# Performance work log

Hardware: AMD Instinct MI355X
Metric: run time of the kernel (lower is better)

## Reference

```python
import jax, jax.numpy as jnp
import numpy as np

PI = float(np.pi)
BN_EPS = 1e-3
LN_EPS = 1e-5


def ssslu(x, shape, bias):
    # x * (sin(softsign(x) * shape*pi/2) + (bias + 1))
    s = x / (1.0 + jnp.abs(x))
    return x * (jnp.sin(s * (shape * PI / 2.0)) + (bias + 1.0))


def bn(x, g, b, m, v):
    inv = (g / jnp.sqrt(v + BN_EPS))[None, :, None, None]
    return (x - m[None, :, None, None]) * inv + b[None, :, None, None]


def conv2d(x, w, bias=None, pad=0):
    y = jax.lax.conv_general_dilated(x, w, (1, 1), [(pad, pad), (pad, pad)],
                                     dimension_numbers=('NCHW', 'OIHW', 'NCHW'))
    if bias is not None:
        y = y + bias[None, :, None, None]
    return y


def ln_silu(v):
    # LayerNorm (unit weight, zero bias) over last axis, then SiLU
    mu = jnp.mean(v, axis=-1, keepdims=True)
    var = jnp.mean(jnp.square(v - mu), axis=-1, keepdims=True)
    h = (v - mu) / jnp.sqrt(var + LN_EPS)
    return h * jax.nn.sigmoid(h)


def _forward(x, w_qkv, g_qkv, b_qkv, m_qkv, v_qkv,
             w_co, g_co, b_co, m_co, v_co,
             w_b1, bias_b1, g_b1, b_b1, m_b1, v_b1,
             w_b2, bias_b2, g_b2, b_b2, m_b2, v_b2):
    B, C, H, W = x.shape
    Q = (w_qkv.shape[0] - C) // 2
    # qkv Conv block: conv1x1 -> SSSLU(-3, 0.3) -> BN
    t = bn(ssslu(conv2d(x, w_qkv, pad=0), -3.0, 0.3), g_qkv, b_qkv, m_qkv, v_qkv)
    xq, xk, xv = jnp.split(t, [Q, 2 * Q], axis=1)
    # max-pooled Q/K rows and columns -> [B*Q, W] / [B*Q, H]
    qw = jnp.max(xq, axis=2).reshape(B * Q, W)
    kw = jnp.max(xk, axis=2).reshape(B * Q, W)
    qh = jnp.max(xq, axis=3).reshape(B * Q, H)
    kh = jnp.max(xk, axis=3).reshape(B * Q, H)
    # xaw[i,b] = max_a qw[i,a]*kw[i,b]; xah[i,a] = max_b qh[i,a]*kh[i,b]
    xaw = jnp.max(qw[:, :, None] * kw[:, None, :], axis=1)  # [BQ, W]
    xah = jnp.max(qh[:, :, None] * kh[:, None, :], axis=2)  # [BQ, H]
    xaw = ln_silu(xaw)
    xah = ln_silu(xah)
    xa = (xah[:, :, None] * xaw[:, None, :]).reshape(B, Q, H, W)
    # co: SSSLUConv(Q+C -> Q): conv3x3 -> BN -> SSSLU(1.0, 0)
    xa = jnp.concatenate([xa, xv], axis=1)
    xa = ssslu(bn(conv2d(xa, w_co, pad=1), g_co, b_co, m_co, v_co), 1.0, 0.0)
    # back[0]: Conv(Q -> C, k3, bias): conv -> SSSLU(-3, 0.3) -> BN
    xa = bn(ssslu(conv2d(xa, w_b1, bias_b1, pad=1), -3.0, 0.3), g_b1, b_b1, m_b1, v_b1)
    # back[1]: SSSLUConv(C -> C, k1, bias): conv -> BN -> SSSLU(0.8, 0)
    xa = ssslu(bn(conv2d(xa, w_b2, bias_b2, pad=0), g_b2, b_b2, m_b2, v_b2), 0.8, 0.0)
    # back[2]: Sigmoid; source returns the gate itself
    return jax.nn.sigmoid(xa)


def setup_inputs() -> dict:
    B, C, Q, H, W = 16, 256, 256, 64, 64
    key = jax.random.key(0)
    ks = jax.random.split(key, 32)

    def w_init(k, o, i, kh, kw):
        return jax.random.normal(k, (o, i, kh, kw), jnp.float32) * (1.0 / np.sqrt(i * kh * kw))

    def bn_params(k, c):
        k1, k2, k3, k4 = jax.random.split(k, 4)
        g = jax.random.uniform(k1, (c,), jnp.float32, 0.5, 1.5)
        b = jax.random.normal(k2, (c,), jnp.float32) * 0.1
        m = jax.random.normal(k3, (c,), jnp.float32) * 0.1
        v = jax.random.uniform(k4, (c,), jnp.float32, 0.5, 1.5)
        return g, b, m, v

    x = jax.random.normal(ks[0], (B, C, H, W), jnp.float32)
    w_qkv = w_init(ks[1], 2 * Q + C, C, 1, 1)
    g_qkv, b_qkv, m_qkv, v_qkv = bn_params(ks[2], 2 * Q + C)
    w_co = w_init(ks[3], Q, Q + C, 3, 3)
    g_co, b_co, m_co, v_co = bn_params(ks[4], Q)
    w_b1 = w_init(ks[5], C, Q, 3, 3)
    bias_b1 = jax.random.normal(ks[6], (C,), jnp.float32) * 0.05
    g_b1, b_b1, m_b1, v_b1 = bn_params(ks[7], C)
    w_b2 = w_init(ks[8], C, C, 1, 1)
    bias_b2 = jax.random.normal(ks[9], (C,), jnp.float32) * 0.05
    g_b2, b_b2, m_b2, v_b2 = bn_params(ks[10], C)
    return dict(x=x, w_qkv=w_qkv, g_qkv=g_qkv, b_qkv=b_qkv, m_qkv=m_qkv, v_qkv=v_qkv,
                w_co=w_co, g_co=g_co, b_co=b_co, m_co=m_co, v_co=v_co,
                w_b1=w_b1, bias_b1=bias_b1, g_b1=g_b1, b_b1=b_b1, m_b1=m_b1, v_b1=v_b1,
                w_b2=w_b2, bias_b2=bias_b2, g_b2=g_b2, b_b2=b_b2, m_b2=m_b2, v_b2=v_b2)


def reference(x, w_qkv, g_qkv, b_qkv, m_qkv, v_qkv,
              w_co, g_co, b_co, m_co, v_co,
              w_b1, bias_b1, g_b1, b_b1, m_b1, v_b1,
              w_b2, bias_b2, g_b2, b_b2, m_b2, v_b2):
    return _forward(x, w_qkv, g_qkv, b_qkv, m_qkv, v_qkv,
                    w_co, g_co, b_co, m_co, v_co,
                    w_b1, bias_b1, g_b1, b_b1, m_b1, v_b1,
                    w_b2, bias_b2, g_b2, b_b2, m_b2, v_b2)
```

## Files before the change

kernel.cpp:

```cpp
#include <hip/hip_runtime.h>
#include <hip/hip_bf16.h>
#include <math.h>

#define PI_F 3.14159265358979323846f

typedef unsigned short u16;
typedef unsigned int   u32;
typedef float    f32x4 __attribute__((ext_vector_type(4)));
typedef _Float16 f16x8 __attribute__((ext_vector_type(8)));
typedef u16      u16x8 __attribute__((ext_vector_type(8)));

__device__ __forceinline__ u16 f2h(float f){ union{ _Float16 h; u16 u; } c; c.h = (_Float16)f; return c.u; }
__device__ __forceinline__ float h2f(u16 u){ union{ u16 u; _Float16 h; } c; c.u = u; return (float)c.h; }

__device__ __forceinline__ void gl16(const void* g, void* l){
  __builtin_amdgcn_global_load_lds((const __attribute__((address_space(1))) u32*)g,
                                   (__attribute__((address_space(3))) u32*)l, 16, 0, 0);
}

__device__ __forceinline__ int SWZ(int r){ return (r>>1)&3; }

__device__ __forceinline__ float wred_max(float v){
#pragma unroll
  for (int m = 32; m; m >>= 1) v = fmaxf(v, __shfl_xor(v, m));
  return v;
}
__device__ __forceinline__ float wred_min(float v){
#pragma unroll
  for (int m = 32; m; m >>= 1) v = fminf(v, __shfl_xor(v, m));
  return v;
}
__device__ __forceinline__ float wred_sum(float v){
#pragma unroll
  for (int m = 32; m; m >>= 1) v += __shfl_xor(v, m);
  return v;
}

__device__ __forceinline__ float ssslu_f(float x, float shp, float bp1){
  float s = x / (1.0f + fabsf(x));
  return x * (__sinf(s * shp) + bp1);
}

__device__ __forceinline__ float epi_val(float v, float4 p, float shp, float bp1, int ORDER, bool SIG){
  v += p.w;
  if (ORDER == 0){ v = ssslu_f(v, shp, bp1); v = (v - p.z) * p.x + p.y; }
  else           { v = (v - p.z) * p.x + p.y; v = ssslu_f(v, shp, bp1); }
  if (SIG) v = 1.f / (1.f + __expf(-v));
  return v;
}

__device__ __forceinline__ void atomicMaxF(float* a, float v){
  if (v >= 0.f) atomicMax(reinterpret_cast<int*>(a), __float_as_int(v));
  else          atomicMin(reinterpret_cast<unsigned int*>(a), __float_as_uint(v));
}

__device__ __forceinline__ f16x8 mul8h(u16x8 a, u16x8 b){
  union{ u16x8 u; f16x8 h; } A, B; A.u = a; B.u = b;
  return A.h * B.h;
}

template<int CI_T, bool CAT>
__global__ __launch_bounds__(512, 2)
void conv3_mfma(const u16* __restrict__ Apk, const u16* __restrict__ Bg,
                u16* __restrict__ DstH, const float4* __restrict__ pp,
                const u16* __restrict__ xahT_, const u16* __restrict__ xawT_,
                float shp, float bp1, int ORDER)
{
  constexpr int NCC = CI_T / 32;
  constexpr int NIT = NCC * 3;
  __shared__ __align__(16) u16 sAB[73728];

  const int tid  = threadIdx.x;
  const int lane = tid & 63;
  const int wv   = tid >> 6;
  const int wm   = wv >> 2;
  const int wn   = wv & 3;
  const int l15  = lane & 15, l4 = lane >> 4;

  const int bx  = blockIdx.x;
  const int bid = (bx & 7) * 32 + (bx >> 3);
  const int b   = bid >> 4;
  const int r0  = (bid & 15) * 4;

  auto STAGE = [&](int it2){
    int d2 = it2 % 3, c2 = it2 / 3;
    if (d2 == 0){
      int bufB = c2 & 1;
#pragma unroll
      for (int j = 0; j < 3; ++j){
        int rr  = 2 * j + (tid >> 8);
        int hh  = r0 - 1 + rr; hh = min(63, max(0, hh));
        int rem = tid & 255;
        int w   = rem >> 2, s = rem & 3;
        int ci0 = c2 * 32 + ((s ^ SWZ(w + 1)) << 3);
        if (CAT && c2 < 8){
          u16x8 vh = *(const u16x8*)&xahT_[((b * 64 + hh) << 8) + ci0];
          u16x8 vw = *(const u16x8*)&xawT_[((b * 64 + w ) << 8) + ci0];
          *(f16x8*)&sAB[49152 + bufB * 12288 + rr * 2048 + w * 32 + s * 8] = mul8h(vh, vw);
        } else {
          int ci = CAT ? (ci0 - 256) : ci0;
          const u16* src = Bg + (((size_t)b * 4096 + hh * 64 + w) << 8) + ci;
          gl16(src, &sAB[49152 + bufB * 12288 + rr * 2048 + (wv & 3) * 512]);
        }
      }
    }
    int bufA = it2 & 1;
#pragma unroll
    for (int j2 = 0; j2 < 3; ++j2){
      int tap = d2 * 3 + j2;
      const u16* base = Apk + (size_t)tap * 256 * CI_T + c2 * 32;
#pragma unroll
      for (int i = 0; i < 2; ++i){
        int row = i * 128 + (tid >> 2);
        int s   = tid & 3;
        const u16* src = base + (size_t)row * CI_T + ((s ^ SWZ(row)) << 3);
        gl16(src, &sAB[bufA * 24576 + j2 * 8192 + (i * 128 + wv * 16) * 32]);
      }
    }
  };

  f32x4 acc[8][4];
#pragma unroll
  for (int i = 0; i < 8; ++i)
#pragma unroll
    for (int j = 0; j < 4; ++j){ acc[i][j][0]=0.f; acc[i][j][1]=0.f; acc[i][j][2]=0.f; acc[i][j][3]=0.f; }

  STAGE(0);
  __syncthreads();

  for (int it = 0; it < NIT; ++it){
    if (it + 1 < NIT) STAGE(it + 1);

    const int d = it % 3, c = it / 3;
    const int bufA = it & 1, bufB = c & 1;
    const int brow = wn + d;
    const bool rowok = ((unsigned)(r0 + wn + d - 1)) < 64u;

#pragma unroll
    for (int dw = 0; dw < 3; ++dw){
      f16x8 afr[8], bfr[4];
#pragma unroll
      for (int fm = 0; fm < 8; ++fm){
        int m  = wm * 128 + fm * 16 + l15;
        int sl = l4 ^ SWZ(m);
        afr[fm] = *(const f16x8*)&sAB[bufA * 24576 + dw * 8192 + m * 32 + sl * 8];
      }
#pragma unroll
      for (int fn = 0; fn < 4; ++fn){
        int w_in = fn * 16 + l15 + dw - 1;
        int wc   = min(63, max(0, w_in));
        int sl2  = l4 ^ SWZ(wc + 1);
        f16x8 t  = *(const f16x8*)&sAB[49152 + bufB * 12288 + brow * 2048 + wc * 32 + sl2 * 8];
        bool ok  = rowok && (((unsigned)w_in) < 64u);
        bfr[fn]  = ok ? t : (f16x8)(_Float16)0;
      }
      __builtin_amdgcn_s_setprio(1);
#pragma unroll
      for (int fm = 0; fm < 8; ++fm)
#pragma unroll
        for (int fn = 0; fn < 4; ++fn)
          acc[fm][fn] = __builtin_amdgcn_mfma_f32_16x16x32_f16(afr[fm], bfr[fn], acc[fm][fn], 0, 0, 0);
      __builtin_amdgcn_s_setprio(0);
    }
    __syncthreads();
  }

  const int h = r0 + wn;
#pragma unroll
  for (int fm = 0; fm < 8; ++fm){
    const int cobase = wm * 128 + fm * 16 + 4 * l4;
    float4 P0 = pp[cobase], P1 = pp[cobase+1], P2 = pp[cobase+2], P3 = pp[cobase+3];
#pragma unroll
    for (int fn = 0; fn < 4; ++fn){
      int w = fn * 16 + l15;
      float v0 = epi_val(acc[fm][fn][0], P0, shp, bp1, ORDER, false);
      float v1 = epi_val(acc[fm][fn][1], P1, shp, bp1, ORDER, false);
      float v2 = epi_val(acc[fm][fn][2], P2, shp, bp1, ORDER, false);
      float v3 = epi_val(acc[fm][fn][3], P3, shp, bp1, ORDER, false);
      uint2 st;
      st.x = (u32)f2h(v0) | ((u32)f2h(v1) << 16);
      st.y = (u32)f2h(v2) | ((u32)f2h(v3) << 16);
      *(uint2*)&DstH[(((size_t)b * 4096 + (size_t)h * 64 + w) << 8) + cobase] = st;
    }
  }
}

template<int SRC, int EPI, int HLOOP>
__global__ __launch_bounds__(256)
void conv_mfma(const u16* __restrict__ Apk, const u16* __restrict__ Bg,
               u16* __restrict__ DstH, float* __restrict__ DstF,
               const float4* __restrict__ pp,
               const float* __restrict__ Xf,
               float* __restrict__ qwp, float* __restrict__ kwp,
               float* __restrict__ qhp, float* __restrict__ khp,
               float shp, float bp1, int ORDER, int M)
{
  constexpr int NCC = 8;
  __shared__ __align__(16) u16 sA[2][8192];
  __shared__ __align__(16) u16 sB[2][2112];

  const int tid  = threadIdx.x;
  const int lane = tid & 63;
  const int wv   = tid >> 6;
  const int bx   = blockIdx.x;
  const int b    = (HLOOP == 8) ? (bx >> 3) : (bx >> 6);
  const int h0   = (HLOOP == 8) ? ((bx & 7) * 8) : (bx & 63);
  const int m0   = blockIdx.y * 256;

  f32x4 acc[4][4];
  f32x4 cmax[4][4];
  if (EPI == 0){
#pragma unroll
    for (int i = 0; i < 4; ++i)
#pragma unroll
      for (int j = 0; j < 4; ++j){ cmax[i][j][0]=-3.0e38f; cmax[i][j][1]=-3.0e38f; cmax[i][j][2]=-3.0e38f; cmax[i][j][3]=-3.0e38f; }
  }

  for (int hi = 0; hi < HLOOP; ++hi){
    const int h = h0 + hi;
#pragma unroll
    for (int i = 0; i < 4; ++i)
#pragma unroll
      for (int j = 0; j < 4; ++j){ acc[i][j][0]=0.f; acc[i][j][1]=0.f; acc[i][j][2]=0.f; acc[i][j][3]=0.f; }

    auto stageA = [&](int c, int buf){
      const u16* base = Apk + (size_t)m0 * 256 + c * 32;
#pragma unroll
      for (int i = 0; i < 4; ++i){
        int row = i * 64 + (tid >> 2);
        int s   = tid & 3;
        const u16* src = base + (size_t)row * 256 + ((s ^ SWZ(row)) << 3);
        gl16(src, &sA[buf][(i * 64 + wv * 16) * 32]);
      }
    };
    auto stageB = [&](int c, int buf){
      const int w = tid >> 2, s = tid & 3, r = w + 1;
      if (SRC == 0){
        int ci0 = c * 32 + ((s ^ SWZ(r)) << 3);
        const float* xp = Xf + ((size_t)(b * 256 + ci0)) * 4096 + h * 64 + w;
        u16x8 v;
#pragma unroll
        for (int j = 0; j < 8; ++j) v[j] = f2h(xp[(size_t)j * 4096]);
        *(u16x8*)&sB[buf][r * 32 + s * 8] = v;
      } else {
        const u16* src = Bg + (((size_t)b * 4096 + h * 64 + w) << 8) + c * 32 + ((s ^ SWZ(r)) << 3);
        gl16(src, &sB[buf][(1 + wv * 16) * 32]);
      }
    };

    __syncthreads();
    stageA(0, 0);
    stageB(0, 0);
    __syncthreads();

    for (int it = 0; it < NCC; ++it){
      if (it + 1 < NCC){ stageA(it + 1, (it + 1) & 1); stageB(it + 1, (it + 1) & 1); }
      f16x8 afr[4], bfr[4];
#pragma unroll
      for (int fm = 0; fm < 4; ++fm){
        int row = wv * 64 + fm * 16 + (lane & 15);
        int sl  = (lane >> 4) ^ SWZ(row);
        afr[fm] = *(const f16x8*)&sA[it & 1][row * 32 + sl * 8];
      }
#pragma unroll
      for (int fn = 0; fn < 4; ++fn){
        int r  = fn * 16 + (lane & 15) + 1;
        int sl = (lane >> 4) ^ SWZ(r);
        bfr[fn] = *(const f16x8*)&sB[it & 1][r * 32 + sl * 8];
      }
      __builtin_amdgcn_s_setprio(1);
#pragma unroll
      for (int fm = 0; fm < 4; ++fm)
#pragma unroll
        for (int fn = 0; fn < 4; ++fn)
          acc[fm][fn] = __builtin_amdgcn_mfma_f32_16x16x32_f16(afr[fm], bfr[fn], acc[fm][fn], 0, 0, 0);
      __builtin_amdgcn_s_setprio(0);
      __syncthreads();
    }

    const int l15 = lane & 15, l4 = lane >> 4;
    if (EPI == 0){
#pragma unroll
      for (int fm = 0; fm < 4; ++fm){
        const int cobase = m0 + wv * 64 + fm * 16 + 4 * l4;
        float4 P0 = pp[cobase], P1 = pp[cobase+1], P2 = pp[cobase+2], P3 = pp[cobase+3];
        f32x4 ev[4];
#pragma unroll
        for (int fn = 0; fn < 4; ++fn){
          ev[fn][0] = epi_val(acc[fm][fn][0], P0, shp, bp1, ORDER, false);
          ev[fn][1] = epi_val(acc[fm][fn][1], P1, shp, bp1, ORDER, false);
          ev[fn][2] = epi_val(acc[fm][fn][2], P2, shp, bp1, ORDER, false);
          ev[fn][3] = epi_val(acc[fm][fn][3], P3, shp, bp1, ORDER, false);
#pragma unroll
          for (int r = 0; r < 4; ++r) cmax[fm][fn][r] = fmaxf(cmax[fm][fn][r], ev[fn][r]);
        }
#pragma unroll
        for (int r = 0; r < 4; ++r){
          float mv = fmaxf(fmaxf(ev[0][r], ev[1][r]), fmaxf(ev[2][r], ev[3][r]));
          mv = fmaxf(mv, __shfl_xor(mv, 1));
          mv = fmaxf(mv, __shfl_xor(mv, 2));
          mv = fmaxf(mv, __shfl_xor(mv, 4));
          mv = fmaxf(mv, __shfl_xor(mv, 8));
          if (l15 == 0){
            int q = (cobase + r) & 255;
            float* rowp = (m0 == 0) ? qhp : khp;
            rowp[(((b << 8) | q) << 6) + h] = mv;
          }
        }
      }
    } else if (EPI == 1){
#pragma unroll
      for (int fm = 0; fm < 4; ++fm){
        const int cobase = wv * 64 + fm * 16 + 4 * l4;
        float4 P0 = pp[cobase], P1 = pp[cobase+1], P2 = pp[cobase+2], P3 = pp[cobase+3];
#pragma unroll
        for (int fn = 0; fn < 4; ++fn){
          int w = fn * 16 + l15;
          float v0 = epi_val(acc[fm][fn][0], P0, shp, bp1, ORDER, false);
          float v1 = epi_val(acc[fm][fn][1], P1, shp, bp1, ORDER, false);
          float v2 = epi_val(acc[fm][fn][2], P2, shp, bp1, ORDER, false);
          float v3 = epi_val(acc[fm][fn][3], P3, shp, bp1, ORDER, false);
          uint2 st;
          st.x = (u32)f2h(v0) | ((u32)f2h(v1) << 16);
          st.y = (u32)f2h(v2) | ((u32)f2h(v3) << 16);
          *(uint2*)&DstH[(((size_t)b * 4096 + (size_t)h * 64 + w) << 8) + cobase] = st;
        }
      }
    } else {
#pragma unroll
      for (int fm = 0; fm < 4; ++fm){
        const int cobase = wv * 64 + fm * 16 + 4 * l4;
        float4 P0 = pp[cobase], P1 = pp[cobase+1], P2 = pp[cobase+2], P3 = pp[cobase+3];
#pragma unroll
        for (int fn = 0; fn < 4; ++fn){
          int w = fn * 16 + l15;
          float v0 = epi_val(acc[fm][fn][0], P0, shp, bp1, ORDER, true);
          float v1 = epi_val(acc[fm][fn][1], P1, shp, bp1, ORDER, true);
          float v2 = epi_val(acc[fm][fn][2], P2, shp, bp1, ORDER, true);
          float v3 = epi_val(acc[fm][fn][3], P3, shp, bp1, ORDER, true);
          size_t base = ((size_t)(b * 256 + cobase)) * 4096 + h * 64 + w;
          DstF[base]          = v0;
          DstF[base + 4096]   = v1;
          DstF[base + 2*4096] = v2;
          DstF[base + 3*4096] = v3;
        }
      }
    }
  }

  if (EPI == 0){
    const int l15 = lane & 15, l4 = lane >> 4;
    float* colp = (m0 == 0) ? qwp : kwp;
#pragma unroll
    for (int fm = 0; fm < 4; ++fm)
#pragma unroll
      for (int fn = 0; fn < 4; ++fn)
#pragma unroll
        for (int r = 0; r < 4; ++r){
          int q = (m0 + wv * 64 + fm * 16 + 4 * l4 + r) & 255;
          int w = fn * 16 + l15;
          atomicMaxF(&colp[(((b << 8) | q) << 6) + w], cmax[fm][fn][r]);
        }
  }
}

__device__ __forceinline__ float ln_silu_wave(float v){
  float mu = wred_sum(v) * (1.f / 64.f);
  float d = v - mu;
  float var = wred_sum(d * d) * (1.f / 64.f);
  float hn = d * rsqrtf(var + 1e-5f);
  return hn / (1.f + __expf(-hn));
}

__global__ void attn_k(const float* __restrict__ qw, const float* __restrict__ kw,
                       const float* __restrict__ qh, const float* __restrict__ kh,
                       u16* __restrict__ xahT, u16* __restrict__ xawT)
{
  int row  = blockIdx.x * 4 + (threadIdx.x >> 6);
  int lane = threadIdx.x & 63;
  int idx  = (row << 6) + lane;
  float qwv = qw[idx], kwv = kw[idx], qhv = qh[idx], khv = kh[idx];
  float Pq = wred_max(qwv), mq = wred_min(qwv);
  float Pk = wred_max(khv), mk = wred_min(khv);
  float aw = fmaxf(kwv * Pq, kwv * mq);
  float ah = fmaxf(qhv * Pk, qhv * mk);
  aw = ln_silu_wave(aw);
  ah = ln_silu_wave(ah);
  int b = row >> 8, q = row & 255;
  xawT[((b * 64 + lane) << 8) + q] = f2h(aw);
  xahT[((b * 64 + lane) << 8) + q] = f2h(ah);
}

__global__ void pack_k(const float* __restrict__ wqkv, const float* __restrict__ wco,
                       const float* __restrict__ wb1, const float* __restrict__ wb2,
                       const float* gq, const float* bq, const float* mq, const float* vq,
                       const float* gc, const float* bc, const float* mc, const float* vc,
                       const float* g1, const float* b1, const float* m1, const float* v1, const float* bias1,
                       const float* g2, const float* b2, const float* m2, const float* v2, const float* bias2,
                       u16* __restrict__ WQ, u16* __restrict__ WCO, u16* __restrict__ WB1, u16* __restrict__ WB2,
                       float4* __restrict__ PP)
{
  const int E0 = 196608, E1 = 196608 + 1179648, E2 = 196608 + 1179648 + 589824, E3 = 2031616;
  int i = blockIdx.x * 256 + threadIdx.x;
  if (i >= E3 + 1536) return;
  if (i < E0){ WQ[i] = f2h(wqkv[i]); }
  else if (i < E1){
    int d = i - E0; int tap = d / 131072; int rm = d % 131072; int m = rm >> 9; int ci = rm & 511;
    WCO[d] = f2h(wco[(size_t)((m << 9) | ci) * 9 + tap]);
  } else if (i < E2){
    int d = i - E1; int tap = d / 65536; int rm = d & 65535; int m = rm >> 8; int ci = rm & 255;
    WB1[d] = f2h(wb1[(size_t)((m << 8) | ci) * 9 + tap]);
  } else if (i < E3){
    int d = i - E2; WB2[d] = f2h(wb2[d]);
  } else {
    int c = i - E3;
    float g, be, mm, vv, bi;
    if (c < 768){ g = gq[c]; be = bq[c]; mm = mq[c]; vv = vq[c]; bi = 0.f; }
    else if (c < 1024){ int j = c - 768;  g = gc[j]; be = bc[j]; mm = mc[j]; vv = vc[j]; bi = 0.f; }
    else if (c < 1280){ int j = c - 1024; g = g1[j]; be = b1[j]; mm = m1[j]; vv = v1[j]; bi = bias1[j]; }
    else              { int j = c - 1280; g = g2[j]; be = b2[j]; mm = m2[j]; vv = v2[j]; bi = bias2[j]; }
    PP[c] = make_float4(g / sqrtf(vv + 1e-3f), be, mm, bi);
  }
}

__global__ void initpool_k(float* __restrict__ p)
{
  int i = blockIdx.x * 1024 + threadIdx.x * 4;
  float4 v = make_float4(-3.0e38f, -3.0e38f, -3.0e38f, -3.0e38f);
  *(float4*)(p + i) = v;
}

extern "C" void kernel_launch(void* const* d_in, const int* in_sizes, int n_in,
                              void* d_out, int out_size, void* d_ws, size_t ws_size,
                              hipStream_t stream)
{
  const float* x       = (const float*)d_in[0];
  const float* w_qkv   = (const float*)d_in[1];
  const float* g_qkv   = (const float*)d_in[2];
  const float* b_qkv   = (const float*)d_in[3];
  const float* m_qkv   = (const float*)d_in[4];
  const float* v_qkv   = (const float*)d_in[5];
  const float* w_co    = (const float*)d_in[6];
  const float* g_co    = (const float*)d_in[7];
  const float* b_co    = (const float*)d_in[8];
  const float* m_co    = (const float*)d_in[9];
  const float* v_co    = (const float*)d_in[10];
  const float* w_b1    = (const float*)d_in[11];
  const float* bias_b1 = (const float*)d_in[12];
  const float* g_b1    = (const float*)d_in[13];
  const float* b_b1    = (const float*)d_in[14];
  const float* m_b1    = (const float*)d_in[15];
  const float* v_b1    = (const float*)d_in[16];
  const float* w_b2    = (const float*)d_in[17];
  const float* bias_b2 = (const float*)d_in[18];
  const float* g_b2    = (const float*)d_in[19];
  const float* b_b2    = (const float*)d_in[20];
  const float* m_b2    = (const float*)d_in[21];
  const float* v_b2    = (const float*)d_in[22];
  float* out = (float*)d_out;

  char* W = (char*)d_ws;
  u16*    WQ   = (u16*)(W + 0);
  u16*    WCO  = (u16*)(W + 393216);
  u16*    WB1  = (u16*)(W + 2752512);
  u16*    WB2  = (u16*)(W + 3932160);
  float4* PP   = (float4*)(W + 4063232);
  u16*    TV   = (u16*)(W + 4087808);
  u16*    XAHT = (u16*)(W + 37642240);
  u16*    XAWT = (u16*)(W + 38166528);
  float*  qw_  = (float*)(W + 38690816);
  float*  kw_  = (float*)(W + 39739392);
  float*  qh_  = (float*)(W + 40787968);
  float*  kh_  = (float*)(W + 41836544);
  u16*    Y1   = (u16*)(W + 38690816);
  u16*    Y2   = TV;

  const size_t NEED = 72245248;
  if (ws_size < NEED) return;

  const float SHP_N3 = -3.0f * PI_F * 0.5f;
  const float SHP_1  =  1.0f * PI_F * 0.5f;
  const float SHP_08 =  0.8f * PI_F * 0.5f;

  dim3 blk(256);

  pack_k<<<7942, blk, 0, stream>>>(w_qkv, w_co, w_b1, w_b2,
      g_qkv, b_qkv, m_qkv, v_qkv,
      g_co,  b_co,  m_co,  v_co,
      g_b1,  b_b1,  m_b1,  v_b1,  bias_b1,
      g_b2,  b_b2,  m_b2,  v_b2,  bias_b2,
      WQ, WCO, WB1, WB2, PP);

  initpool_k<<<512, blk, 0, stream>>>(qw_);

  conv_mfma<0, 0, 8><<<dim3(128, 2), blk, 0, stream>>>(
      WQ, nullptr, nullptr, nullptr, PP, x,
      qw_, kw_, qh_, kh_, SHP_N3, 1.3f, 0, 512);

  conv_mfma<0, 1, 1><<<dim3(1024, 1), blk, 0, stream>>>(
      WQ + (size_t)512 * 256, nullptr, TV, nullptr, PP + 512, x,
      nullptr, nullptr, nullptr, nullptr, SHP_N3, 1.3f, 0, 256);

  attn_k<<<1024, blk, 0, stream>>>(qw_, kw_, qh_, kh_, XAHT, XAWT);

  conv3_mfma<512, true><<<256, 512, 0, stream>>>(
      WCO, TV, Y1, PP + 768, XAHT, XAWT, SHP_1, 1.0f, 1);

  conv3_mfma<256, false><<<256, 512, 0, stream>>>(
      WB1, Y1, Y2, PP + 1024, nullptr, nullptr, SHP_N3, 1.3f, 0);

  conv_mfma<1, 2, 1><<<dim3(1024, 1), blk, 0, stream>>>(
      WB2, Y2, nullptr, out, PP + 1280, nullptr,
      nullptr, nullptr, nullptr, nullptr, SHP_08, 1.0f, 1, 256);
}
```

Measured before the change: 442.4 us.

## Pre-transpose input to fp16 channel-last once and reuse for both qkv convs

Adds a transpose kernel that converts the NCHW fp32 input to an fp16 NHWC buffer once. Both qkv 1x1 conv launches then read that buffer through the SRC=1 path instead of converting fp32 x themselves. The Q/K conv also moves from 8 rows per block to 4, doubling its grid, and the pooling buffers are relocated so they do not overlap the new XH buffer. The cost is an extra launch plus a larger workspace requirement, traded for cheaper and better-coalesced operand loads in the convs.

```diff
diff --git a/kernel.cpp b/kernel.cpp
--- a/kernel.cpp
+++ b/kernel.cpp
@@ -9,6 +9,7 @@
 typedef float    f32x4 __attribute__((ext_vector_type(4)));
 typedef _Float16 f16x8 __attribute__((ext_vector_type(8)));
 typedef u16      u16x8 __attribute__((ext_vector_type(8)));
+typedef u16      u16x4 __attribute__((ext_vector_type(4)));
 
 __device__ __forceinline__ u16 f2h(float f){ union{ _Float16 h; u16 u; } c; c.h = (_Float16)f; return c.u; }
 __device__ __forceinline__ float h2f(u16 u){ union{ u16 u; _Float16 h; } c; c.u = u; return (float)c.h; }
@@ -57,6 +58,40 @@
 __device__ __forceinline__ f16x8 mul8h(u16x8 a, u16x8 b){
   union{ u16x8 u; f16x8 h; } A, B; A.u = a; B.u = b;
   return A.h * B.h;
+}
+
+__global__ __launch_bounds__(256)
+void xpose_k(const float* __restrict__ X, u16* __restrict__ XH)
+{
+  __shared__ u16 L[16384];
+  const int tid = threadIdx.x;
+  const int b = blockIdx.x >> 6, h = blockIdx.x & 63;
+  const float* xp = X + (size_t)b * 256 * 4096 + h * 64;
+#pragma unroll
+  for (int i = 0; i < 16; ++i){
+    int ci = i * 16 + (tid >> 4);
+    int w4 = (tid & 15) * 4;
+    float4 v = *(const float4*)(xp + (size_t)ci * 4096 + w4);
+    int sw = 4 * ((ci >> 3) & 15);
+    u16x4 d;
+    d[0] = f2h(v.x); d[1] = f2h(v.y); d[2] = f2h(v.z); d[3] = f2h(v.w);
+    *(u16x4*)&L[ci * 64 + (w4 ^ sw)] = d;
+  }
+  __syncthreads();
+  u16* out = XH + (((size_t)b * 4096 + (size_t)h * 64) << 8);
+#pragma unroll
+  for (int it = 0; it < 8; ++it){
+    int w   = it * 8 + (tid >> 5);
+    int m   = tid & 31;
+    int ci0 = m * 8;
+    int base = (w & ~3) ^ (4 * (m & 15));
+    int wl   = w & 3;
+    u16x8 o;
+#pragma unroll
+    for (int k = 0; k < 8; ++k)
+      o[k] = L[(ci0 + k) * 64 + base + wl];
+    *(u16x8*)&out[w * 256 + ci0] = o;
+  }
 }
 
 template<int CI_T, bool CAT>
@@ -196,6 +231,7 @@
                float shp, float bp1, int ORDER, int M)
 {
   constexpr int NCC = 8;
+  constexpr int HG  = 64 / HLOOP;
   __shared__ __align__(16) u16 sA[2][8192];
   __shared__ __align__(16) u16 sB[2][2112];
 
@@ -203,8 +239,8 @@
   const int lane = tid & 63;
   const int wv   = tid >> 6;
   const int bx   = blockIdx.x;
-  const int b    = (HLOOP == 8) ? (bx >> 3) : (bx >> 6);
-  const int h0   = (HLOOP == 8) ? ((bx & 7) * 8) : (bx & 63);
+  const int b    = bx / HG;
+  const int h0   = (bx % HG) * HLOOP;
   const int m0   = blockIdx.y * 256;
 
   f32x4 acc[4][4];
@@ -468,14 +504,15 @@
   u16*    TV   = (u16*)(W + 4087808);
   u16*    XAHT = (u16*)(W + 37642240);
   u16*    XAWT = (u16*)(W + 38166528);
-  float*  qw_  = (float*)(W + 38690816);
-  float*  kw_  = (float*)(W + 39739392);
-  float*  qh_  = (float*)(W + 40787968);
-  float*  kh_  = (float*)(W + 41836544);
+  u16*    XH   = (u16*)(W + 38690816);
   u16*    Y1   = (u16*)(W + 38690816);
   u16*    Y2   = TV;
-
-  const size_t NEED = 72245248;
+  float*  qw_  = (float*)(W + 72245248);
+  float*  kw_  = (float*)(W + 73293824);
+  float*  qh_  = (float*)(W + 74342400);
+  float*  kh_  = (float*)(W + 75390976);
+
+  const size_t NEED = 76439552;
   if (ws_size < NEED) return;
 
   const float SHP_N3 = -3.0f * PI_F * 0.5f;
@@ -493,12 +530,14 @@
 
   initpool_k<<<512, blk, 0, stream>>>(qw_);
 
-  conv_mfma<0, 0, 8><<<dim3(128, 2), blk, 0, stream>>>(
-      WQ, nullptr, nullptr, nullptr, PP, x,
+  xpose_k<<<1024, blk, 0, stream>>>(x, XH);
+
+  conv_mfma<1, 0, 4><<<dim3(256, 2), blk, 0, stream>>>(
+      WQ, XH, nullptr, nullptr, PP, nullptr,
       qw_, kw_, qh_, kh_, SHP_N3, 1.3f, 0, 512);
 
-  conv_mfma<0, 1, 1><<<dim3(1024, 1), blk, 0, stream>>>(
-      WQ + (size_t)512 * 256, nullptr, TV, nullptr, PP + 512, x,
+  conv_mfma<1, 1, 1><<<dim3(1024, 1), blk, 0, stream>>>(
+      WQ + (size_t)512 * 256, XH, TV, nullptr, PP + 512, nullptr,
       nullptr, nullptr, nullptr, nullptr, SHP_N3, 1.3f, 0, 256);
 
   attn_k<<<1024, blk, 0, stream>>>(qw_, kw_, qh_, kh_, XAHT, XAWT);
```

Measured after the change: 452.9 us. 2.4% more time.
